# Kernel tuning notes

Measured on AMD Instinct MI355X. Metric: run time of the kernel, lower is better.

The kernel has to match this reference:

```python
import jax, jax.numpy as jnp
import numpy as np

N, K, C0, H = 256, 16, 16, 32  # vertices, regular degree, input feats, hidden


def setup_inputs() -> dict:
    key = jax.random.key(0)
    ks = jax.random.split(key, 4)
    # k-regular circulant graph: neighbors of i are i+/-1..i+/-K//2 (mod N), sorted by vertex id
    offs = np.concatenate([np.arange(1, K // 2 + 1), -np.arange(1, K // 2 + 1)])
    nbrs = np.sort((np.arange(N)[:, None] + offs[None, :]) % N, axis=1).astype(np.int32)
    X = jax.random.normal(ks[0], (N, C0), jnp.float32)
    W1 = jax.random.normal(ks[1], (18 * C0, H), jnp.float32) / np.sqrt(18 * C0)
    b1 = jnp.zeros((H,), jnp.float32)
    W2 = jax.random.normal(ks[2], (18 * H, H), jnp.float32) / np.sqrt(18 * H)
    b2 = jnp.zeros((H,), jnp.float32)
    fc_w = jax.random.normal(ks[3], (H, 1), jnp.float32) / np.sqrt(H)
    fc_b = jnp.zeros((1,), jnp.float32)
    return {"X": X, "nbrs": jnp.asarray(nbrs), "W1": W1, "b1": b1,
            "W2": W2, "b2": b2, "fc_w": fc_w, "fc_b": fc_b}


def contract18(T, A):
    """All 18 contractions of F6[t,a,b,e,f,c] = T[t,a,b,c] * A[e,f],
    exactly matching _collapse6to3 (_c6to2_111 + _c6to2_12 + _c6to2_3),
    without materializing the 6-d tensor.
    T: (n, k, k, k, c) with axes (vertex, t, a, b, channel); A: (k, k).
    Returns (n, k, k, 18*c)."""
    S = A.sum()            # total sum of A
    r = A.sum(1)           # row sums
    tr = jnp.trace(A)
    sum_b = T.sum(3)              # (n,t,a,c)
    sum_t = T.sum(1)              # (n,a,b,c)
    sum_ab = T.sum((2, 3))        # (n,t,c)
    sum_tb = T.sum((1, 3))        # (n,a,c)
    sum_all = T.sum((1, 2, 3))    # (n,c)
    # _c6to2_111 (5 permutations)
    c1 = sum_b * S
    c2 = sum_ab[:, :, None, :] * r[None, None, :, None]
    c3 = sum_t * S
    c4 = sum_tb[:, :, None, :] * r[None, None, :, None]
    c5 = sum_all[:, None, None, :] * A[None, :, :, None]
    # _c6to2_12 (1 nontrivial permutation + 9 identical identity permutations)
    c6 = jnp.einsum('ntabc,b->ntac', T, r)
    c7 = sum_b * tr  # repeated 9 times, as in the source
    # _c6to2_3 (3 planar-diagonal contractions)
    d_ab = jnp.diagonal(T, axis1=2, axis2=3).transpose(0, 1, 3, 2)   # (n,t,a,c): T[t,a,a,c]
    c16 = jnp.einsum('ntac,ea->ntec', d_ab, A)
    d_tb = jnp.diagonal(T, axis1=1, axis2=3)                          # (n,a,c,t): T[t,a,t,c]
    c17 = jnp.einsum('nact,et->naec', d_tb, A)
    d_ttt = jnp.einsum('ntttc->ntc', T).sum(1)                        # (n,c)
    c18 = d_ttt[:, None, None, :] * A[None, :, :, None]
    return jnp.concatenate([c1, c2, c3, c4, c5, c6] + [c7] * 9 + [c16, c17, c18], axis=-1)


def _forward(X, nbrs, W1, b1, W2, b2, fc_w, fc_b):
    n, k = nbrs.shape
    # chi_{i,t}[a,p] = 1 iff a-th neighbor of i == p-th neighbor of j, j = nbrs[i,t]
    NN = nbrs[nbrs]                                                    # (n,k,k)
    CH = (nbrs[:, None, :, None] == NN[:, :, None, :]).astype(X.dtype)  # (n,t,a,p)
    A = jnp.eye(k, dtype=X.dtype)  # chi_{i,i} is the k x k identity for every i

    # get_F0: broadcast vertex features to (n, k, k, c0)
    F = jnp.broadcast_to(X[:, None, None, :], (n, k, k, X.shape[1]))

    def layer(F, W, b):
        Fg = F[nbrs]                                             # (n,t,p,q,c) gather neighbor features
        tmp = jnp.einsum('ntap,ntpqc->ntaqc', CH, Fg)            # chi @ F
        T = jnp.einsum('ntaqc,ntbq->ntabc', tmp, CH)             # (chi @ F) @ chi^T
        col = contract18(T, A)                                   # (n,k,k,18c)
        return jax.nn.relu(col @ W + b)

    F1 = layer(F, W1, b1)
    F2 = layer(F1, W2, b2)
    # get_Troot then full sum: chi_root scatters F2 entries injectively into [n,n,c],
    # so sum over Troot == sum over all entries of F2.
    g = F2.sum((0, 1, 2))                                        # (H,)
    return g @ fc_w + fc_b                                       # (1,)


def reference(X, nbrs, W1, b1, W2, b2, fc_w, fc_b):
    return _forward(X, nbrs, W1, b1, W2, b2, fc_w, fc_b)
```

## Files before the change

### kernel.cpp

```cpp
#include <hip/hip_runtime.h>


constexpr int KN = 16, HH = 32, NV = 256, C2 = 32;

__device__ __forceinline__ float rlane(float v, int l) {
    return __int_as_float(__builtin_amdgcn_readlane(__float_as_int(v), l));
}

#define MM_RL(WPTR, NB, COEF_EXPR, ACC) do {                                   \
    _Pragma("unroll")                                                          \
    for (int B = 0; B < (NB); ++B) {                                           \
        const float4 w_ = ((const float4*)(WPTR))[B * 64 + lane];              \
        _Pragma("unroll")                                                      \
        for (int cc = 0; cc < 8; ++cc) {                                       \
            const int ci = B * 8 + cc;                                         \
            const float cf_ = (COEF_EXPR);                                     \
            _Pragma("unroll")                                                  \
            for (int h4 = 0; h4 < 8; ++h4) {                                   \
                const int src_ = 8 * cc + h4;                                  \
                (ACC)[4*h4+0] = fmaf(cf_, rlane(w_.x, src_), (ACC)[4*h4+0]);   \
                (ACC)[4*h4+1] = fmaf(cf_, rlane(w_.y, src_), (ACC)[4*h4+1]);   \
                (ACC)[4*h4+2] = fmaf(cf_, rlane(w_.z, src_), (ACC)[4*h4+2]);   \
                (ACC)[4*h4+3] = fmaf(cf_, rlane(w_.w, src_), (ACC)[4*h4+3]);   \
            }                                                                  \
        }                                                                      \
    }                                                                          \
} while (0)

__global__ __launch_bounds__(512, 2)
void ccn_l1(const float* __restrict__ X, const int* __restrict__ nbrs,
            const float* __restrict__ W1, const float* __restrict__ bias,
            float* __restrict__ F1c, float* __restrict__ outz)
{
    __shared__ float sE1[6 * 512];
    __shared__ float sPP[256 * 36];
    __shared__ float sX[16][20];
    __shared__ float sV[16][164];
    __shared__ int   s_nbi[16];
    __shared__ int   s_nbj[16][17];
    __shared__ int   s_P[16][16];
    __shared__ int   s_vm[16];
    __shared__ float s_m[16];

    const int tid  = threadIdx.x;
    const int i    = ((blockIdx.x & 7) << 5) | (blockIdx.x >> 3);
    const int lane = tid & 63;

    if (blockIdx.x == 0 && tid == 0) outz[0] = 0.f;
    if (tid < 16) s_nbi[tid] = nbrs[i * 16 + tid];
    __syncthreads();

    if (tid < 256) {
        const int t = tid >> 4, y = tid & 15;
        const int j = s_nbi[t];
        s_nbj[t][y] = nbrs[j * 16 + y];
        sX[t][y]    = X[j * 16 + y];
    } else {
        const int u = tid - 256;
        float acc = 0.f;
        #pragma unroll
        for (int g = 6; g < 15; ++g) acc += W1[g * 512 + u];
        sE1[u]        = 16.f * W1[u] + W1[5 * 512 + u] + 16.f * acc;
        sE1[512 + u]  = W1[512 + u];
        sE1[1024 + u] = W1[15 * 512 + u];
        sE1[1536 + u] = 16.f * W1[2 * 512 + u];
        sE1[2048 + u] = W1[3 * 512 + u];
        sE1[2560 + u] = W1[4 * 512 + u];
    }
    __syncthreads();

    if (tid < 256) {
        const int t = tid >> 4, y = tid & 15;
        const int tgt = s_nbi[y];
        int p = -1;
        #pragma unroll
        for (int q = 0; q < 16; ++q) if (s_nbj[t][q] == tgt) p = q;
        s_P[t][y] = p;
        unsigned long long bal = __ballot(p >= 0);
        if (y == 0) {
            int vm = (int)((bal >> ((t & 3) * 16)) & 0xFFFFull);
            s_vm[t] = vm;
            s_m[t]  = (float)__popc(vm);
        }
    } else {
        const int u = tid;
        float acc = 0.f;
        #pragma unroll
        for (int g = 6; g < 15; ++g) acc += W1[g * 512 + u];
        sE1[u]        = 16.f * W1[u] + W1[5 * 512 + u] + 16.f * acc;
        sE1[512 + u]  = W1[512 + u];
        sE1[1024 + u] = W1[15 * 512 + u];
        sE1[1536 + u] = 16.f * W1[2 * 512 + u];
        sE1[2048 + u] = W1[3 * 512 + u];
        sE1[2560 + u] = W1[4 * 512 + u];
    }
    __syncthreads();

    if (tid < 256) {
        const int t = tid >> 4, y = tid & 15, x = t;
        float Y0[16];
        #pragma unroll
        for (int c4 = 0; c4 < 4; ++c4) {
            float4 v = *(const float4*)&sX[t][4 * c4];
            Y0[4*c4+0] = v.x; Y0[4*c4+1] = v.y; Y0[4*c4+2] = v.z; Y0[4*c4+3] = v.w;
        }
        float Z4[16], Z5[16];
        #pragma unroll
        for (int c = 0; c < 16; ++c) { Z4[c] = 0.f; Z5[c] = 0.f; }
        #pragma unroll
        for (int tp = 0; tp < 16; ++tp) {
            const int vm = s_vm[tp];
            const float mt = s_m[tp];
            const float fb = ((vm >> x) & 1) ? mt : 0.f;
            const float f5 = mt * mt;
            #pragma unroll
            for (int c4 = 0; c4 < 4; ++c4) {
                float4 v = *(const float4*)&sX[tp][4 * c4];
                Z4[4*c4+0] = fmaf(fb, v.x, Z4[4*c4+0]);
                Z4[4*c4+1] = fmaf(fb, v.y, Z4[4*c4+1]);
                Z4[4*c4+2] = fmaf(fb, v.z, Z4[4*c4+2]);
                Z4[4*c4+3] = fmaf(fb, v.w, Z4[4*c4+3]);
                Z5[4*c4+0] = fmaf(f5, v.x, Z5[4*c4+0]);
                Z5[4*c4+1] = fmaf(f5, v.y, Z5[4*c4+1]);
                Z5[4*c4+2] = fmaf(f5, v.z, Z5[4*c4+2]);
                Z5[4*c4+3] = fmaf(f5, v.w, Z5[4*c4+3]);
            }
        }
        const float m = s_m[t];
        float v0a=0.f,v0b=0.f,v1a=0.f,v1b=0.f,v2a=0.f,v2b=0.f;
        float v3a=0.f,v3b=0.f,v4a=0.f,v4b=0.f;
        const float2* Wsb = (const float2*)(sE1 + 0 * 512);
        const float2* Wab = (const float2*)(sE1 + 1 * 512);
        const float2* W16 = (const float2*)(sE1 + 2 * 512);
        const float2* Wtb = (const float2*)(sE1 + 4 * 512);
        const float2* Wal = (const float2*)(sE1 + 5 * 512);
        #pragma unroll
        for (int c = 0; c < 16; ++c) {
            const float cf0 = m * Y0[c];
            const float cf1 = m * cf0;
            const float cf2 = Y0[c];
            const float cf3 = Z4[c];
            const float cf4 = Z5[c];
            const int idx = c * 16 + y;
            float2 w0 = Wsb[idx]; v0a = fmaf(cf0, w0.x, v0a); v0b = fmaf(cf0, w0.y, v0b);
            float2 w1 = Wab[idx]; v1a = fmaf(cf1, w1.x, v1a); v1b = fmaf(cf1, w1.y, v1b);
            float2 w2 = W16[idx]; v2a = fmaf(cf2, w2.x, v2a); v2b = fmaf(cf2, w2.y, v2b);
            float2 w3 = Wtb[idx]; v3a = fmaf(cf3, w3.x, v3a); v3b = fmaf(cf3, w3.y, v3b);
            float2 w4 = Wal[idx]; v4a = fmaf(cf4, w4.x, v4a); v4b = fmaf(cf4, w4.y, v4b);
        }
        *(float2*)&sV[t][0 * 32 + 2 * y] = make_float2(v0a, v0b);
        *(float2*)&sV[t][1 * 32 + 2 * y] = make_float2(v1a, v1b);
        *(float2*)&sV[t][2 * 32 + 2 * y] = make_float2(v2a, v2b);
        *(float2*)&sV[t][3 * 32 + 2 * y] = make_float2(v3a, v3b);
        *(float2*)&sV[t][4 * 32 + 2 * y] = make_float2(v4a, v4b);
    } else {
        const int w = tid - 256;
        const int t = w >> 4, y = w & 15, x = t;
        float Z2[16];
        #pragma unroll
        for (int c = 0; c < 16; ++c) Z2[c] = 0.f;
        #pragma unroll
        for (int tp = 0; tp < 16; ++tp) {
            const int vm = s_vm[tp];
            const float f2 = (float)((vm >> x) & (vm >> y) & 1);
            #pragma unroll
            for (int c4 = 0; c4 < 4; ++c4) {
                float4 v = *(const float4*)&sX[tp][4 * c4];
                Z2[4*c4+0] = fmaf(f2, v.x, Z2[4*c4+0]);
                Z2[4*c4+1] = fmaf(f2, v.y, Z2[4*c4+1]);
                Z2[4*c4+2] = fmaf(f2, v.z, Z2[4*c4+2]);
                Z2[4*c4+3] = fmaf(f2, v.w, Z2[4*c4+3]);
            }
        }
        float pp[HH];
        #pragma unroll
        for (int h = 0; h < HH; ++h) pp[h] = 0.f;
        MM_RL(sE1 + 3 * 512, 2, Z2[ci], pp);
        float* dst = &sPP[(t * 16 + y) * 36];
        #pragma unroll
        for (int h4 = 0; h4 < 8; ++h4)
            *(float4*)&dst[4 * h4] = make_float4(pp[4*h4], pp[4*h4+1], pp[4*h4+2], pp[4*h4+3]);
    }
    __syncthreads();

    float fr[HH];
    if (tid < 256) {
        const int t = tid >> 4, y = tid & 15, x = t;
        const float vy  = (s_P[t][y] >= 0) ? 1.f : 0.f;
        const float dxy = (x == y) ? 1.f : 0.f;
        const float* pp = &sPP[(t * 16 + y) * 36];
        #pragma unroll
        for (int h4 = 0; h4 < 8; ++h4) {
            const float4 V0 = *(const float4*)&sV[t][0 * 32 + 4 * h4];
            const float4 V1 = *(const float4*)&sV[t][1 * 32 + 4 * h4];
            const float4 V2 = *(const float4*)&sV[t][2 * 32 + 4 * h4];
            const float4 V3 = *(const float4*)&sV[t][3 * 32 + 4 * h4];
            const float4 V4 = *(const float4*)&sV[t][4 * 32 + 4 * h4];
            const float4 PP = *(const float4*)&pp[4 * h4];
            float a_ = vy*(V0.x+V2.x) + V1.x + V3.x + dxy*V4.x + PP.x + bias[4*h4+0];
            float b_ = vy*(V0.y+V2.y) + V1.y + V3.y + dxy*V4.y + PP.y + bias[4*h4+1];
            float c_ = vy*(V0.z+V2.z) + V1.z + V3.z + dxy*V4.z + PP.z + bias[4*h4+2];
            float d_ = vy*(V0.w+V2.w) + V1.w + V3.w + dxy*V4.w + PP.w + bias[4*h4+3];
            fr[4*h4+0] = a_ > 0.f ? a_ : 0.f;
            fr[4*h4+1] = b_ > 0.f ? b_ : 0.f;
            fr[4*h4+2] = c_ > 0.f ? c_ : 0.f;
            fr[4*h4+3] = d_ > 0.f ? d_ : 0.f;
        }
    }
    __syncthreads();

    if (tid < 256) {
        const int t = tid >> 4, y = tid & 15;
        float* dst = &sPP[(y * 16 + t) * 36];
        #pragma unroll
        for (int h4 = 0; h4 < 8; ++h4)
            *(float4*)&dst[4 * h4] = make_float4(fr[4*h4], fr[4*h4+1], fr[4*h4+2], fr[4*h4+3]);
    }
    __syncthreads();

    if (tid < 256) {
        const int q = tid >> 4, p = tid & 15;
        const float* src = &sPP[(q * 16 + p) * 36];
        float4* F4 = (float4*)F1c;
        const size_t basec = ((size_t)i * 16 + q) * 128 + p;
        #pragma unroll
        for (int c4 = 0; c4 < 8; ++c4)
            F4[basec + c4 * 16] = *(const float4*)&src[4 * c4];
    }
}

__global__ __launch_bounds__(512, 2)
void ccn_l2(const float* __restrict__ F1c, const int* __restrict__ nbrs,
            const float* __restrict__ W2, const float* __restrict__ bias,
            const float* __restrict__ fcw, const float* __restrict__ fcb,
            float* __restrict__ out)
{
    __shared__ float sE2[6 * 1024];
    __shared__ float sRpp[256 * 36];
    __shared__ float s_stb[16 * 33];
    __shared__ float s_sall[C2];
    __shared__ int   s_nbi[16];
    __shared__ int   s_PQ[16 * 17];
    __shared__ float s_red[4];

    const int tid  = threadIdx.x;
    const int i    = ((blockIdx.x & 7) << 5) | (blockIdx.x >> 3);
    const int lane = tid & 63;
    const float4* F4 = (const float4*)F1c;

    if (tid < 16) s_nbi[tid] = nbrs[i * 16 + tid];
    __syncthreads();

    if (tid < 256) {
        const int t = tid >> 4, y = tid & 15;
        const int j = s_nbi[t];
        s_PQ[t * 17 + y] = nbrs[j * 16 + y];
    } else {
        const int w = tid - 256;
        #pragma unroll
        for (int k = 0; k < 2; ++k) {
            const int u = w + k * 256;
            float acc = 0.f;
            #pragma unroll
            for (int g = 6; g < 15; ++g) acc += W2[g * 1024 + u];
            sE2[u]        = 16.f * W2[u] + W2[5 * 1024 + u] + 16.f * acc;
            sE2[1024 + u] = W2[1024 + u];
            sE2[2048 + u] = W2[15 * 1024 + u];
            sE2[3072 + u] = 16.f * W2[2 * 1024 + u];
            sE2[4096 + u] = W2[3 * 1024 + u];
            sE2[5120 + u] = W2[4 * 1024 + u];
        }
    }
    __syncthreads();

    if (tid < 256) {
        const int t = tid >> 4, y = tid & 15;
        const int tgt = s_nbi[y];
        int p = -1;
        #pragma unroll
        for (int q = 0; q < 16; ++q) if (s_PQ[t * 17 + q] == tgt) p = q;
        s_PQ[t * 17 + y] = p;
    } else {
        const int w = tid - 256;
        #pragma unroll
        for (int k = 2; k < 4; ++k) {
            const int u = w + k * 256;
            float acc = 0.f;
            #pragma unroll
            for (int g = 6; g < 15; ++g) acc += W2[g * 1024 + u];
            sE2[u]        = 16.f * W2[u] + W2[5 * 1024 + u] + 16.f * acc;
            sE2[1024 + u] = W2[1024 + u];
            sE2[2048 + u] = W2[15 * 1024 + u];
            sE2[3072 + u] = 16.f * W2[2 * 1024 + u];
            sE2[4096 + u] = W2[3 * 1024 + u];
            sE2[5120 + u] = W2[4 * 1024 + u];
        }
    }
    __syncthreads();

    float pre[HH];
    float sab[C2];
    float pp[HH];

    if (tid < 256) {
        const int t = tid >> 4, y = tid & 15;
        const int j = s_nbi[t];
        const int p = s_PQ[t * 17 + y];
        const float mp = (p >= 0) ? 1.f : 0.f;
        const int pc = p >= 0 ? p : 0;
        const size_t jbase = (size_t)j * 2048;

        float R[C2];
        #pragma unroll
        for (int c = 0; c < C2; ++c) R[c] = 0.f;
        #pragma unroll
        for (int b = 0; b < 16; ++b) {
            const int q = s_PQ[t * 17 + b];
            const float mm = (q >= 0) ? mp : 0.f;
            const int qc = q >= 0 ? q : 0;
            const size_t rb = jbase + (size_t)qc * 128 + pc;
            #pragma unroll
            for (int c4 = 0; c4 < 8; ++c4) {
                float4 v = F4[rb + c4 * 16];
                R[4*c4+0] = fmaf(mm, v.x, R[4*c4+0]);
                R[4*c4+1] = fmaf(mm, v.y, R[4*c4+1]);
                R[4*c4+2] = fmaf(mm, v.z, R[4*c4+2]);
                R[4*c4+3] = fmaf(mm, v.w, R[4*c4+3]);
            }
        }
        #pragma unroll
        for (int c4 = 0; c4 < 8; ++c4)
            *(float4*)&sRpp[(t * 16 + y) * 36 + 4 * c4] =
                make_float4(R[4*c4+0], R[4*c4+1], R[4*c4+2], R[4*c4+3]);

        #pragma unroll
        for (int h = 0; h < HH; ++h) pre[h] = 0.f;
        MM_RL(sE2 + 0 * 1024, 4, R[ci], pre);

        #pragma unroll
        for (int c = 0; c < C2; ++c) {
            float s = R[c];
            s += __shfl_xor(s, 1);
            s += __shfl_xor(s, 2);
            s += __shfl_xor(s, 4);
            s += __shfl_xor(s, 8);
            sab[c] = s;
        }

        float D[C2];
        {
            const size_t db = jbase + (size_t)pc * 128 + pc;
            #pragma unroll
            for (int c4 = 0; c4 < 8; ++c4) {
                float4 v = F4[db + c4 * 16];
                D[4*c4+0] = mp * v.x; D[4*c4+1] = mp * v.y;
                D[4*c4+2] = mp * v.z; D[4*c4+3] = mp * v.w;
            }
        }
        MM_RL(sE2 + 2 * 1024, 4, D[ci], pre);
    } else {
        const int w = tid - 256;
        const int g = w >> 4, l = w & 15;
        float ST[C2];
        #pragma unroll
        for (int c = 0; c < C2; ++c) ST[c] = 0.f;
        #pragma unroll
        for (int tp = 0; tp < 16; ++tp) {
            const int jt = s_nbi[tp];
            const int py = s_PQ[tp * 17 + g];
            const int px = s_PQ[tp * 17 + l];
            const float mm = (px >= 0 && py >= 0) ? 1.f : 0.f;
            const int pyc = py >= 0 ? py : 0;
            const int pxc = px >= 0 ? px : 0;
            const size_t rb = (size_t)jt * 2048 + (size_t)pyc * 128 + pxc;
            #pragma unroll
            for (int c4 = 0; c4 < 8; ++c4) {
                float4 v = F4[rb + c4 * 16];
                ST[4*c4+0] = fmaf(mm, v.x, ST[4*c4+0]);
                ST[4*c4+1] = fmaf(mm, v.y, ST[4*c4+1]);
                ST[4*c4+2] = fmaf(mm, v.z, ST[4*c4+2]);
                ST[4*c4+3] = fmaf(mm, v.w, ST[4*c4+3]);
            }
        }
        #pragma unroll
        for (int h = 0; h < HH; ++h) pp[h] = 0.f;
        MM_RL(sE2 + 3 * 1024, 4, ST[ci], pp);
    }
    __syncthreads();

    if (tid < 256) {
        #pragma unroll
        for (int k = 0; k < 2; ++k) {
            const int x2 = (tid >> 5) + 8 * k;
            const int c = tid & 31;
            float s = 0.f;
            #pragma unroll
            for (int tt = 0; tt < 16; ++tt) s += sRpp[(tt * 16 + x2) * 36 + c];
            s_stb[x2 * 33 + c] = s;
        }
    }
    __syncthreads();

    if (tid < 256) {
        if (tid < 32) {
            float s = 0.f;
            #pragma unroll
            for (int x2 = 0; x2 < 16; ++x2) s += s_stb[x2 * 33 + tid];
            s_sall[tid] = s;
        }
    } else {
        const int w = tid - 256;
        const int g = w >> 4, l = w & 15;
        float* dst = &sRpp[(l * 16 + g) * 36];
        #pragma unroll
        for (int h4 = 0; h4 < 8; ++h4)
            *(float4*)&dst[4 * h4] = make_float4(pp[4*h4], pp[4*h4+1], pp[4*h4+2], pp[4*h4+3]);
    }
    __syncthreads();

    if (tid < 256) {
        const int t = tid >> 4, y = tid & 15, x = t;
        const float dxy = (x == y) ? 1.f : 0.f;
        float S0 = 0.f, S1 = 0.f, L0 = 0.f, L1 = 0.f;
        {
            const float2* Wab = (const float2*)(sE2 + 1 * 1024);
            const float2* Wtb = (const float2*)(sE2 + 4 * 1024);
            const float2* Wal = (const float2*)(sE2 + 5 * 1024);
            #pragma unroll
            for (int c = 0; c < C2; ++c) {
                const float cfa = sab[c];
                const float cft = s_stb[t * 33 + c];
                const float cfl = s_sall[c];
                const int idx = c * 16 + y;
                float2 wa = Wab[idx]; S0 = fmaf(cfa, wa.x, S0); S1 = fmaf(cfa, wa.y, S1);
                float2 wt = Wtb[idx]; S0 = fmaf(cft, wt.x, S0); S1 = fmaf(cft, wt.y, S1);
                float2 wl = Wal[idx]; L0 = fmaf(cfl, wl.x, L0); L1 = fmaf(cfl, wl.y, L1);
            }
        }
        const int gbase = (t & 3) * 16;
        #pragma unroll
        for (int h = 0; h < HH; ++h) {
            const int src = gbase + (h >> 1);
            const float sv = (h & 1) ? S1 : S0;
            const float lv = (h & 1) ? L1 : L0;
            pre[h] += __shfl(sv, src, 64) + dxy * __shfl(lv, src, 64);
        }
        {
            const float* ppr = &sRpp[(t * 16 + y) * 36];
            #pragma unroll
            for (int h4 = 0; h4 < 8; ++h4) {
                const float4 v = *(const float4*)&ppr[4 * h4];
                pre[4*h4+0] += v.x; pre[4*h4+1] += v.y;
                pre[4*h4+2] += v.z; pre[4*h4+3] += v.w;
            }
        }
        float local = 0.f;
        #pragma unroll
        for (int h = 0; h < HH; ++h) {
            float v = pre[h] + bias[h];
            v = v > 0.f ? v : 0.f;
            local += v * fcw[h];
        }
        #pragma unroll
        for (int off = 32; off > 0; off >>= 1) local += __shfl_down(local, off, 64);
        if (lane == 0) s_red[tid >> 6] = local;
    }
    __syncthreads();
    if (tid == 0) {
        const float v = s_red[0] + s_red[1] + s_red[2] + s_red[3]
                      + fcb[0] * (1.f / 256.f);
        atomicAdd(out, v);
    }
}

extern "C" void kernel_launch(void* const* d_in, const int* in_sizes, int n_in,
                              void* d_out, int out_size, void* d_ws, size_t ws_size,
                              hipStream_t stream) {
    const float* X    = (const float*)d_in[0];
    const int*   nbrs = (const int*)  d_in[1];
    const float* W1   = (const float*)d_in[2];
    const float* b1   = (const float*)d_in[3];
    const float* W2   = (const float*)d_in[4];
    const float* b2   = (const float*)d_in[5];
    const float* fc_w = (const float*)d_in[6];
    const float* fc_b = (const float*)d_in[7];
    float* outp = (float*)d_out;

    float* F1c = (float*)d_ws;

    ccn_l1<<<NV, 512, 0, stream>>>(X, nbrs, W1, b1, F1c, outp);
    ccn_l2<<<NV, 512, 0, stream>>>(F1c, nbrs, W2, b2, fc_w, fc_b, outp);
}
```

Measured before the change: 108.3 us.

## Split layer-2 channels across both thread halves and precompute W2 reductions once

Before this change, layer 2 split its threads by role: half gathered rows and diagonals, the other half gathered the transposed sums. Now every cell is handled by both 256-thread halves, each covering 16 of the 32 channels, so all 512 threads do gather and matmul work. The per-block W2 reduction into effective weights moves into a small separate prep kernel that writes to workspace, and layer 2 reads those weights from global memory instead of shared. This trades extra barriers, an extra kernel launch and cross-half partial-sum reductions through shared memory for better load balance and less redundant weight preprocessing.

```diff
diff --git a/kernel.cpp b/kernel.cpp
--- a/kernel.cpp
+++ b/kernel.cpp
@@ -7,25 +7,45 @@
     return __int_as_float(__builtin_amdgcn_readlane(__float_as_int(v), l));
 }
 
-#define MM_RL(WPTR, NB, COEF_EXPR, ACC) do {                                   \
-    _Pragma("unroll")                                                          \
-    for (int B = 0; B < (NB); ++B) {                                           \
-        const float4 w_ = ((const float4*)(WPTR))[B * 64 + lane];              \
-        _Pragma("unroll")                                                      \
-        for (int cc = 0; cc < 8; ++cc) {                                       \
-            const int ci = B * 8 + cc;                                         \
-            const float cf_ = (COEF_EXPR);                                     \
-            _Pragma("unroll")                                                  \
-            for (int h4 = 0; h4 < 8; ++h4) {                                   \
-                const int src_ = 8 * cc + h4;                                  \
-                (ACC)[4*h4+0] = fmaf(cf_, rlane(w_.x, src_), (ACC)[4*h4+0]);   \
-                (ACC)[4*h4+1] = fmaf(cf_, rlane(w_.y, src_), (ACC)[4*h4+1]);   \
-                (ACC)[4*h4+2] = fmaf(cf_, rlane(w_.z, src_), (ACC)[4*h4+2]);   \
-                (ACC)[4*h4+3] = fmaf(cf_, rlane(w_.w, src_), (ACC)[4*h4+3]);   \
-            }                                                                  \
-        }                                                                      \
-    }                                                                          \
-} while (0)
+__device__ __forceinline__ void mmrl16(const float* __restrict__ Wg,
+                                       const float* cfrow, int lane,
+                                       float* acc) {
+    const float4 w0 = ((const float4*)Wg)[lane];
+    const float4 w1 = ((const float4*)Wg)[64 + lane];
+    #pragma unroll 1
+    for (int B = 0; B < 2; ++B) {
+        const float4 w_ = (B == 0) ? w0 : w1;
+        float cf[8];
+        #pragma unroll
+        for (int cc = 0; cc < 8; ++cc) cf[cc] = cfrow[B * 8 + cc];
+        #pragma unroll
+        for (int cc = 0; cc < 8; ++cc) {
+            #pragma unroll
+            for (int h4 = 0; h4 < 8; ++h4) {
+                const int src = 8 * cc + h4;
+                acc[4*h4+0] = fmaf(cf[cc], rlane(w_.x, src), acc[4*h4+0]);
+                acc[4*h4+1] = fmaf(cf[cc], rlane(w_.y, src), acc[4*h4+1]);
+                acc[4*h4+2] = fmaf(cf[cc], rlane(w_.z, src), acc[4*h4+2]);
+                acc[4*h4+3] = fmaf(cf[cc], rlane(w_.w, src), acc[4*h4+3]);
+            }
+        }
+    }
+}
+
+__global__ __launch_bounds__(256)
+void ccn_prep(const float* __restrict__ W2, float* __restrict__ E2g)
+{
+    const int u = blockIdx.x * 256 + threadIdx.x;
+    float acc = 0.f;
+    #pragma unroll
+    for (int g = 6; g < 15; ++g) acc += W2[g * 1024 + u];
+    E2g[u]        = 16.f * W2[u] + W2[5 * 1024 + u] + 16.f * acc;
+    E2g[1024 + u] = W2[1024 + u];
+    E2g[2048 + u] = W2[15 * 1024 + u];
+    E2g[3072 + u] = 16.f * W2[2 * 1024 + u];
+    E2g[4096 + u] = W2[3 * 1024 + u];
+    E2g[5120 + u] = W2[4 * 1024 + u];
+}
 
 __global__ __launch_bounds__(512, 2)
 void ccn_l1(const float* __restrict__ X, const int* __restrict__ nbrs,
@@ -175,7 +195,25 @@
         float pp[HH];
         #pragma unroll
         for (int h = 0; h < HH; ++h) pp[h] = 0.f;
-        MM_RL(sE1 + 3 * 512, 2, Z2[ci], pp);
+        {
+            const float* Wp = sE1 + 3 * 512;
+            #pragma unroll
+            for (int B = 0; B < 2; ++B) {
+                const float4 w_ = ((const float4*)Wp)[B * 64 + lane];
+                #pragma unroll
+                for (int cc = 0; cc < 8; ++cc) {
+                    const float cf_ = Z2[B * 8 + cc];
+                    #pragma unroll
+                    for (int h4 = 0; h4 < 8; ++h4) {
+                        const int src_ = 8 * cc + h4;
+                        pp[4*h4+0] = fmaf(cf_, rlane(w_.x, src_), pp[4*h4+0]);
+                        pp[4*h4+1] = fmaf(cf_, rlane(w_.y, src_), pp[4*h4+1]);
+                        pp[4*h4+2] = fmaf(cf_, rlane(w_.z, src_), pp[4*h4+2]);
+                        pp[4*h4+3] = fmaf(cf_, rlane(w_.w, src_), pp[4*h4+3]);
+                    }
+                }
+            }
+        }
         float* dst = &sPP[(t * 16 + y) * 36];
         #pragma unroll
         for (int h4 = 0; h4 < 8; ++h4)
@@ -231,14 +269,14 @@
 
 __global__ __launch_bounds__(512, 2)
 void ccn_l2(const float* __restrict__ F1c, const int* __restrict__ nbrs,
-            const float* __restrict__ W2, const float* __restrict__ bias,
+            const float* __restrict__ E2g, const float* __restrict__ bias,
             const float* __restrict__ fcw, const float* __restrict__ fcb,
             float* __restrict__ out)
 {
-    __shared__ float sE2[6 * 1024];
-    __shared__ float sRpp[256 * 36];
+    __shared__ float sCf[256 * 33];
     __shared__ float s_stb[16 * 33];
-    __shared__ float s_sall[C2];
+    __shared__ float s_sall[32];
+    __shared__ float sMv[2][16][68];
     __shared__ int   s_nbi[16];
     __shared__ int   s_PQ[16 * 17];
     __shared__ float s_red[4];
@@ -246,220 +284,182 @@
     const int tid  = threadIdx.x;
     const int i    = ((blockIdx.x & 7) << 5) | (blockIdx.x >> 3);
     const int lane = tid & 63;
+    const int h    = tid >> 8;
+    const int cell = tid & 255;
+    const int t = cell >> 4, y = cell & 15;
+    const int hc = 4 * h;
     const float4* F4 = (const float4*)F1c;
 
     if (tid < 16) s_nbi[tid] = nbrs[i * 16 + tid];
     __syncthreads();
-
-    if (tid < 256) {
-        const int t = tid >> 4, y = tid & 15;
-        const int j = s_nbi[t];
-        s_PQ[t * 17 + y] = nbrs[j * 16 + y];
-    } else {
-        const int w = tid - 256;
-        #pragma unroll
-        for (int k = 0; k < 2; ++k) {
-            const int u = w + k * 256;
-            float acc = 0.f;
-            #pragma unroll
-            for (int g = 6; g < 15; ++g) acc += W2[g * 1024 + u];
-            sE2[u]        = 16.f * W2[u] + W2[5 * 1024 + u] + 16.f * acc;
-            sE2[1024 + u] = W2[1024 + u];
-            sE2[2048 + u] = W2[15 * 1024 + u];
-            sE2[3072 + u] = 16.f * W2[2 * 1024 + u];
-            sE2[4096 + u] = W2[3 * 1024 + u];
-            sE2[5120 + u] = W2[4 * 1024 + u];
-        }
-    }
-    __syncthreads();
-
-    if (tid < 256) {
-        const int t = tid >> 4, y = tid & 15;
+    if (tid < 256) s_PQ[t * 17 + y] = nbrs[s_nbi[t] * 16 + y];
+    __syncthreads();
+    if (tid < 256) {
         const int tgt = s_nbi[y];
         int p = -1;
         #pragma unroll
         for (int q = 0; q < 16; ++q) if (s_PQ[t * 17 + q] == tgt) p = q;
         s_PQ[t * 17 + y] = p;
-    } else {
-        const int w = tid - 256;
-        #pragma unroll
-        for (int k = 2; k < 4; ++k) {
-            const int u = w + k * 256;
-            float acc = 0.f;
-            #pragma unroll
-            for (int g = 6; g < 15; ++g) acc += W2[g * 1024 + u];
-            sE2[u]        = 16.f * W2[u] + W2[5 * 1024 + u] + 16.f * acc;
-            sE2[1024 + u] = W2[1024 + u];
-            sE2[2048 + u] = W2[15 * 1024 + u];
-            sE2[3072 + u] = 16.f * W2[2 * 1024 + u];
-            sE2[4096 + u] = W2[3 * 1024 + u];
-            sE2[5120 + u] = W2[4 * 1024 + u];
-        }
-    }
-    __syncthreads();
-
-    float pre[HH];
-    float sab[C2];
-    float pp[HH];
-
-    if (tid < 256) {
-        const int t = tid >> 4, y = tid & 15;
-        const int j = s_nbi[t];
-        const int p = s_PQ[t * 17 + y];
-        const float mp = (p >= 0) ? 1.f : 0.f;
-        const int pc = p >= 0 ? p : 0;
-        const size_t jbase = (size_t)j * 2048;
-
-        float R[C2];
-        #pragma unroll
-        for (int c = 0; c < C2; ++c) R[c] = 0.f;
-        #pragma unroll
-        for (int b = 0; b < 16; ++b) {
-            const int q = s_PQ[t * 17 + b];
-            const float mm = (q >= 0) ? mp : 0.f;
-            const int qc = q >= 0 ? q : 0;
-            const size_t rb = jbase + (size_t)qc * 128 + pc;
-            #pragma unroll
-            for (int c4 = 0; c4 < 8; ++c4) {
-                float4 v = F4[rb + c4 * 16];
-                R[4*c4+0] = fmaf(mm, v.x, R[4*c4+0]);
-                R[4*c4+1] = fmaf(mm, v.y, R[4*c4+1]);
-                R[4*c4+2] = fmaf(mm, v.z, R[4*c4+2]);
-                R[4*c4+3] = fmaf(mm, v.w, R[4*c4+3]);
-            }
-        }
-        #pragma unroll
-        for (int c4 = 0; c4 < 8; ++c4)
-            *(float4*)&sRpp[(t * 16 + y) * 36 + 4 * c4] =
-                make_float4(R[4*c4+0], R[4*c4+1], R[4*c4+2], R[4*c4+3]);
-
-        #pragma unroll
-        for (int h = 0; h < HH; ++h) pre[h] = 0.f;
-        MM_RL(sE2 + 0 * 1024, 4, R[ci], pre);
-
-        #pragma unroll
-        for (int c = 0; c < C2; ++c) {
-            float s = R[c];
-            s += __shfl_xor(s, 1);
-            s += __shfl_xor(s, 2);
-            s += __shfl_xor(s, 4);
-            s += __shfl_xor(s, 8);
-            sab[c] = s;
-        }
-
-        float D[C2];
-        {
-            const size_t db = jbase + (size_t)pc * 128 + pc;
-            #pragma unroll
-            for (int c4 = 0; c4 < 8; ++c4) {
-                float4 v = F4[db + c4 * 16];
-                D[4*c4+0] = mp * v.x; D[4*c4+1] = mp * v.y;
-                D[4*c4+2] = mp * v.z; D[4*c4+3] = mp * v.w;
-            }
-        }
-        MM_RL(sE2 + 2 * 1024, 4, D[ci], pre);
-    } else {
-        const int w = tid - 256;
-        const int g = w >> 4, l = w & 15;
-        float ST[C2];
-        #pragma unroll
-        for (int c = 0; c < C2; ++c) ST[c] = 0.f;
-        #pragma unroll
-        for (int tp = 0; tp < 16; ++tp) {
-            const int jt = s_nbi[tp];
-            const int py = s_PQ[tp * 17 + g];
-            const int px = s_PQ[tp * 17 + l];
-            const float mm = (px >= 0 && py >= 0) ? 1.f : 0.f;
-            const int pyc = py >= 0 ? py : 0;
-            const int pxc = px >= 0 ? px : 0;
-            const size_t rb = (size_t)jt * 2048 + (size_t)pyc * 128 + pxc;
-            #pragma unroll
-            for (int c4 = 0; c4 < 8; ++c4) {
-                float4 v = F4[rb + c4 * 16];
-                ST[4*c4+0] = fmaf(mm, v.x, ST[4*c4+0]);
-                ST[4*c4+1] = fmaf(mm, v.y, ST[4*c4+1]);
-                ST[4*c4+2] = fmaf(mm, v.z, ST[4*c4+2]);
-                ST[4*c4+3] = fmaf(mm, v.w, ST[4*c4+3]);
-            }
-        }
-        #pragma unroll
-        for (int h = 0; h < HH; ++h) pp[h] = 0.f;
-        MM_RL(sE2 + 3 * 1024, 4, ST[ci], pp);
-    }
-    __syncthreads();
-
-    if (tid < 256) {
-        #pragma unroll
-        for (int k = 0; k < 2; ++k) {
-            const int x2 = (tid >> 5) + 8 * k;
-            const int c = tid & 31;
-            float s = 0.f;
-            #pragma unroll
-            for (int tt = 0; tt < 16; ++tt) s += sRpp[(tt * 16 + x2) * 36 + c];
-            s_stb[x2 * 33 + c] = s;
-        }
-    }
-    __syncthreads();
-
-    if (tid < 256) {
-        if (tid < 32) {
-            float s = 0.f;
-            #pragma unroll
-            for (int x2 = 0; x2 < 16; ++x2) s += s_stb[x2 * 33 + tid];
-            s_sall[tid] = s;
-        }
-    } else {
-        const int w = tid - 256;
-        const int g = w >> 4, l = w & 15;
-        float* dst = &sRpp[(l * 16 + g) * 36];
-        #pragma unroll
-        for (int h4 = 0; h4 < 8; ++h4)
-            *(float4*)&dst[4 * h4] = make_float4(pp[4*h4], pp[4*h4+1], pp[4*h4+2], pp[4*h4+3]);
-    }
-    __syncthreads();
-
-    if (tid < 256) {
-        const int t = tid >> 4, y = tid & 15, x = t;
-        const float dxy = (x == y) ? 1.f : 0.f;
+    }
+    __syncthreads();
+
+    const int j = s_nbi[t];
+    const int p = s_PQ[t * 17 + y];
+    const float mp = (p >= 0) ? 1.f : 0.f;
+    const int pc = p >= 0 ? p : 0;
+    const size_t jbase = (size_t)j * 2048;
+    float* myrow = &sCf[cell * 33 + 16 * h];
+
+    float R16[16];
+    #pragma unroll
+    for (int k = 0; k < 16; ++k) R16[k] = 0.f;
+    #pragma unroll
+    for (int b = 0; b < 16; ++b) {
+        const int q = s_PQ[t * 17 + b];
+        const float mm = (q >= 0) ? mp : 0.f;
+        const int qc = q >= 0 ? q : 0;
+        const size_t rb = jbase + (size_t)qc * 128 + hc * 16 + pc;
+        #pragma unroll
+        for (int k = 0; k < 4; ++k) {
+            float4 v = F4[rb + k * 16];
+            R16[4*k+0] = fmaf(mm, v.x, R16[4*k+0]);
+            R16[4*k+1] = fmaf(mm, v.y, R16[4*k+1]);
+            R16[4*k+2] = fmaf(mm, v.z, R16[4*k+2]);
+            R16[4*k+3] = fmaf(mm, v.w, R16[4*k+3]);
+        }
+    }
+    float sab16[16];
+    #pragma unroll
+    for (int k = 0; k < 16; ++k) {
+        float s = R16[k];
+        s += __shfl_xor(s, 1); s += __shfl_xor(s, 2);
+        s += __shfl_xor(s, 4); s += __shfl_xor(s, 8);
+        sab16[k] = s;
+    }
+    #pragma unroll
+    for (int k = 0; k < 16; ++k) myrow[k] = R16[k];
+    __syncthreads();
+
+    float pre[32];
+    #pragma unroll
+    for (int k = 0; k < 32; ++k) pre[k] = 0.f;
+    mmrl16(E2g + 0 * 1024 + h * 512, myrow, lane, pre);
+    {
+        const int x2 = tid >> 5, c = tid & 31;
+        float s = 0.f;
+        #pragma unroll 4
+        for (int tt = 0; tt < 16; ++tt) s += sCf[(tt * 16 + x2) * 33 + c];
+        s_stb[x2 * 33 + c] = s;
+    }
+    __syncthreads();
+
+    if (tid < 32) {
+        float s = 0.f;
+        #pragma unroll
+        for (int x2 = 0; x2 < 16; ++x2) s += s_stb[x2 * 33 + tid];
+        s_sall[tid] = s;
+    }
+    float ST16[16];
+    #pragma unroll
+    for (int k = 0; k < 16; ++k) ST16[k] = 0.f;
+    #pragma unroll
+    for (int tp = 0; tp < 16; ++tp) {
+        const int jt = s_nbi[tp];
+        const int px = s_PQ[tp * 17 + y];
+        const int pq = s_PQ[tp * 17 + t];
+        const float mm = (px >= 0 && pq >= 0) ? 1.f : 0.f;
+        const int pxc = px >= 0 ? px : 0;
+        const int pqc = pq >= 0 ? pq : 0;
+        const size_t rb = (size_t)jt * 2048 + (size_t)pqc * 128 + hc * 16 + pxc;
+        #pragma unroll
+        for (int k = 0; k < 4; ++k) {
+            float4 v = F4[rb + k * 16];
+            ST16[4*k+0] = fmaf(mm, v.x, ST16[4*k+0]);
+            ST16[4*k+1] = fmaf(mm, v.y, ST16[4*k+1]);
+            ST16[4*k+2] = fmaf(mm, v.z, ST16[4*k+2]);
+            ST16[4*k+3] = fmaf(mm, v.w, ST16[4*k+3]);
+        }
+    }
+    float preT[32];
+    #pragma unroll
+    for (int k = 0; k < 32; ++k) preT[k] = 0.f;
+    #pragma unroll
+    for (int k = 0; k < 16; ++k) myrow[k] = ST16[k];
+    mmrl16(E2g + 3 * 1024 + h * 512, myrow, lane, preT);
+    {
+        const size_t db = jbase + (size_t)pc * 128 + hc * 16 + pc;
+        #pragma unroll
+        for (int k = 0; k < 4; ++k) {
+            float4 v = F4[db + k * 16];
+            myrow[4*k+0] = mp * v.x; myrow[4*k+1] = mp * v.y;
+            myrow[4*k+2] = mp * v.z; myrow[4*k+3] = mp * v.w;
+        }
+    }
+    mmrl16(E2g + 2 * 1024 + h * 512, myrow, lane, pre);
+    #pragma unroll
+    for (int k = 0; k < 16; ++k) myrow[k] = sab16[k];
+    __syncthreads();
+
+    {
         float S0 = 0.f, S1 = 0.f, L0 = 0.f, L1 = 0.f;
-        {
-            const float2* Wab = (const float2*)(sE2 + 1 * 1024);
-            const float2* Wtb = (const float2*)(sE2 + 4 * 1024);
-            const float2* Wal = (const float2*)(sE2 + 5 * 1024);
-            #pragma unroll
-            for (int c = 0; c < C2; ++c) {
-                const float cfa = sab[c];
-                const float cft = s_stb[t * 33 + c];
-                const float cfl = s_sall[c];
-                const int idx = c * 16 + y;
-                float2 wa = Wab[idx]; S0 = fmaf(cfa, wa.x, S0); S1 = fmaf(cfa, wa.y, S1);
-                float2 wt = Wtb[idx]; S0 = fmaf(cft, wt.x, S0); S1 = fmaf(cft, wt.y, S1);
-                float2 wl = Wal[idx]; L0 = fmaf(cfl, wl.x, L0); L1 = fmaf(cfl, wl.y, L1);
-            }
-        }
-        const int gbase = (t & 3) * 16;
-        #pragma unroll
-        for (int h = 0; h < HH; ++h) {
-            const int src = gbase + (h >> 1);
-            const float sv = (h & 1) ? S1 : S0;
-            const float lv = (h & 1) ? L1 : L0;
-            pre[h] += __shfl(sv, src, 64) + dxy * __shfl(lv, src, 64);
-        }
-        {
-            const float* ppr = &sRpp[(t * 16 + y) * 36];
-            #pragma unroll
-            for (int h4 = 0; h4 < 8; ++h4) {
-                const float4 v = *(const float4*)&ppr[4 * h4];
-                pre[4*h4+0] += v.x; pre[4*h4+1] += v.y;
-                pre[4*h4+2] += v.z; pre[4*h4+3] += v.w;
-            }
-        }
+        const float2* Wab = (const float2*)(E2g + 1 * 1024);
+        const float2* Wtb = (const float2*)(E2g + 4 * 1024);
+        const float2* Wal = (const float2*)(E2g + 5 * 1024);
+        #pragma unroll 4
+        for (int k = 0; k < 16; ++k) {
+            const int c = 16 * h + k;
+            const float cfa = myrow[k];
+            const float cft = s_stb[t * 33 + c];
+            const float cfl = s_sall[c];
+            const float2 wa = Wab[c * 16 + y];
+            const float2 wt = Wtb[c * 16 + y];
+            const float2 wl = Wal[c * 16 + y];
+            S0 += cfa * wa.x + cft * wt.x;
+            S1 += cfa * wa.y + cft * wt.y;
+            L0 += cfl * wl.x;
+            L1 += cfl * wl.y;
+        }
+        sMv[h][t][2 * y]      = S0;
+        sMv[h][t][2 * y + 1]  = S1;
+        sMv[h][t][32 + 2 * y] = L0;
+        sMv[h][t][33 + 2 * y] = L1;
+    }
+    __syncthreads();
+
+    const int rT = y * 16 + t;
+    if (h == 0) {
+        #pragma unroll
+        for (int k = 0; k < 32; ++k) sCf[rT * 33 + k] = preT[k];
+    }
+    __syncthreads();
+    if (h == 1) {
+        #pragma unroll
+        for (int k = 0; k < 32; ++k) sCf[rT * 33 + k] += preT[k];
+    }
+    __syncthreads();
+    if (h == 0) {
+        #pragma unroll
+        for (int k = 0; k < 32; ++k) pre[k] += sCf[cell * 33 + k];
+    }
+    __syncthreads();
+    if (h == 1) {
+        #pragma unroll
+        for (int k = 0; k < 32; ++k) sCf[cell * 33 + k] = pre[k];
+    }
+    __syncthreads();
+
+    if (h == 0) {
+        #pragma unroll
+        for (int k = 0; k < 32; ++k) pre[k] += sCf[cell * 33 + k];
+        const float dxy = (t == y) ? 1.f : 0.f;
         float local = 0.f;
         #pragma unroll
-        for (int h = 0; h < HH; ++h) {
-            float v = pre[h] + bias[h];
+        for (int k = 0; k < 32; ++k) {
+            const float S = sMv[0][t][k]      + sMv[1][t][k];
+            const float L = sMv[0][t][32 + k] + sMv[1][t][32 + k];
+            float v = pre[k] + S + dxy * L + bias[k];
             v = v > 0.f ? v : 0.f;
-            local += v * fcw[h];
+            local += v * fcw[k];
         }
         #pragma unroll
         for (int off = 32; off > 0; off >>= 1) local += __shfl_down(local, off, 64);
@@ -467,9 +467,8 @@
     }
     __syncthreads();
     if (tid == 0) {
-        const float v = s_red[0] + s_red[1] + s_red[2] + s_red[3]
-                      + fcb[0] * (1.f / 256.f);
-        atomicAdd(out, v);
+        atomicAdd(out, s_red[0] + s_red[1] + s_red[2] + s_red[3]
+                       + fcb[0] * (1.f / 256.f));
     }
 }
 
@@ -487,7 +486,9 @@
     float* outp = (float*)d_out;
 
     float* F1c = (float*)d_ws;
-
+    float* E2g = F1c + (size_t)NV * KN * KN * HH;
+
+    ccn_prep<<<4, 256, 0, stream>>>(W2, E2g);
     ccn_l1<<<NV, 512, 0, stream>>>(X, nbrs, W1, b1, F1c, outp);
-    ccn_l2<<<NV, 512, 0, stream>>>(F1c, nbrs, W2, b2, fc_w, fc_b, outp);
-}
+    ccn_l2<<<NV, 512, 0, stream>>>(F1c, nbrs, E2g, b2, fc_w, fc_b, outp);
+}
```

Result: slower. 113.9 us (+5.2%).
